# Optimization experiments

Measured on AMD Instinct MI355X. Metric: run time of the kernel, lower is better.

Reference implementation:

```python
import jax, jax.numpy as jnp
import numpy as np

D = 32        # number of TT cores (d)
R = 16        # tt_rank
B = 262144    # batch size


def setup_inputs() -> dict:
    key = jax.random.key(0)
    k1, k2, k3, k4 = jax.random.split(key, 4)
    return {
        "X": jax.random.randint(k1, (B, D), 0, 2, dtype=jnp.int32),
        "core_first": jax.random.normal(k2, (1, R, 2), dtype=jnp.float32),
        "cores_mid": jax.random.normal(k3, (D - 2, R, R, 2), dtype=jnp.float32),
        "core_last": jax.random.normal(k4, (R, 1, 2), dtype=jnp.float32),
    }


def reference(X, core_first, cores_mid, core_last):
    # First core: cores[0][:, :, X[:,0]] -> [1, R, B] -> permute -> [B, 1, R].
    # We carry the squeezed [B, R] row vector instead of [B, 1, R].
    carry0 = jnp.take(core_first[0], X[:, 0], axis=-1).T  # [B, R]

    def step(carry, inp):
        core, idx = inp                       # core: [R, R, 2], idx: [B]
        c = jnp.take(core, idx, axis=2)       # gathered core: [R, R, B]
        new = jnp.einsum('br,rsb->bs', carry, c)  # batched (1xR)@(RxR)
        return new, None

    # Middle cores i = 1 .. D-2 (sequential chain, data-dependent).
    carry, _ = jax.lax.scan(step, carry0, (cores_mid, X[:, 1:D - 1].T))

    # Last core: cores[-1][:, :, X[:,-1]] -> [R, 1, B]; contract to scalar per batch.
    c_last = jnp.take(core_last[:, 0, :], X[:, -1], axis=-1)  # [R, B]
    out = jnp.einsum('br,rb->b', carry, c_last)               # [B]  (squeeze of [B,1,1])
    return out
```

## Files before the change

kernel.cpp:

```cpp
#include <hip/hip_runtime.h>


#define R 16
#define TT_D 32
#define BATCH 262144

#define OFF_V16  0
#define OFF_W16  1048576
#define WS_FLOATS 2097152

#define MSTRIDE 268
#define VSTRIDE 17

__device__ __forceinline__ void rowvec_mat(const float* __restrict__ M,
                                           float* __restrict__ u) {
    float nv[R];
    #pragma unroll
    for (int s = 0; s < R; s++) nv[s] = 0.f;
    #pragma unroll
    for (int t2 = 0; t2 < R; t2++) {
        const float a = u[t2];
        #pragma unroll
        for (int s = 0; s < R; s++) nv[s] += a * M[t2 * 16 + s];
    }
    #pragma unroll
    for (int s = 0; s < R; s++) u[s] = nv[s];
}

__device__ __forceinline__ void mat_colvec(const float* __restrict__ M,
                                           float* __restrict__ w) {
    float nw[R];
    #pragma unroll
    for (int r2 = 0; r2 < R; r2++) {
        float a = 0.f;
        #pragma unroll
        for (int k = 0; k < R; k++) a += M[r2 * 16 + k] * w[k];
        nw[r2] = a;
    }
    #pragma unroll
    for (int r2 = 0; r2 < R; r2++) w[r2] = nw[r2];
}

__device__ __forceinline__ void chain4_row(const float* __restrict__ scm, int lbase,
                                           int e, int r, float* __restrict__ u) {
    const float* M0 = scm + lbase * 512 + ((e >> 3) & 1) * 256;
    #pragma unroll
    for (int s = 0; s < R; s++) u[s] = M0[r * 16 + s];
    for (int k = 1; k <= 3; k++) {
        const float* M = scm + (lbase + k) * 512 + ((e >> (3 - k)) & 1) * 256;
        rowvec_mat(M, u);
    }
}

__global__ __launch_bounds__(256) void tt_build(const float* __restrict__ cf,
                                                const float* __restrict__ cm,
                                                const float* __restrict__ cl,
                                                float* __restrict__ ws) {
    __shared__ float scm[15 * 512];
    __shared__ float T0[16 * MSTRIDE];
    __shared__ float T1[16 * MSTRIDE];
    __shared__ float SA[16 * VSTRIDE];
    __shared__ float SE[16 * VSTRIDE];
    __shared__ float SV[16];
    __shared__ float SG[256];

    const int t = threadIdx.x;
    const int e = t >> 4, r = t & 15;
    const bool isPrefix = (blockIdx.x < 256);
    const int h = isPrefix ? blockIdx.x : (blockIdx.x - 256);

    {
        const float2* cm2 = (const float2*)(cm + (isPrefix ? 0 : 15) * 512);
        for (int j = t; j < 15 * 256; j += 256) {
            const float2 vv = cm2[j];
            const int ci = j >> 8, idx = j & 255;
            scm[ci * 512 + idx] = vv.x;
            scm[ci * 512 + 256 + idx] = vv.y;
        }
    }
    __syncthreads();

    if (isPrefix) {
        if (t < 16) {
            SV[t] = cf[t * 2 + ((h >> 7) & 1)];
            for (int j = 0; j < 7; j++) {
                const float* M = scm + j * 512 + (((h >> (6 - j)) & 1) << 8);
                float a = 0.f;
                #pragma unroll
                for (int t2 = 0; t2 < R; t2++) a += SV[t2] * M[t2 * 16 + t];
                SV[t] = a;
            }
        }
        {
            float u[R];
            for (int tab = 0; tab < 2; tab++) {
                chain4_row(scm, 7 + 4 * tab, e, r, u);
                float* dst = (tab ? T1 : T0) + e * MSTRIDE + r * 16;
                #pragma unroll
                for (int s = 0; s < R; s++) dst[s] = u[s];
            }
        }
        __syncthreads();
        float v[R];
        #pragma unroll
        for (int k = 0; k < R; k++) v[k] = SV[k];
        const float* src = T0 + (t >> 4) * MSTRIDE;
        for (int q = 0; q < 2; q++) {
            rowvec_mat(src, v);
            src = T1 + (t & 15) * MSTRIDE;
        }
        float* o = ws + OFF_V16 + (size_t)(h * 256 + t) * 16;
        #pragma unroll
        for (int s = 0; s < R; s++) o[s] = v[s];
    } else {
        {
            float u[R];
            for (int job = 0; job < 2; job++) {
                int lb, ee, rr;
                float* dst;
                bool active = true;
                if (job == 0)      { lb = 8; ee = e;      rr = r;      dst = T0 + e * MSTRIDE + r * 16; }
                else if (t < 16)   { lb = 0; ee = h >> 4; rr = t;      dst = SA + t * VSTRIDE; }
                else if (t < 32)   { lb = 4; ee = h & 15; rr = t - 16; dst = SE + (t - 16) * VSTRIDE; }
                else               { active = false; lb = 0; ee = 0; rr = 0; dst = nullptr; }
                if (active) {
                    chain4_row(scm, lb, ee, rr, u);
                    #pragma unroll
                    for (int s = 0; s < R; s++) dst[s] = u[s];
                }
            }
        }
        if (t >= 48 && t < 64) {
            const int l = t - 48;
            float w[R];
            #pragma unroll
            for (int r2 = 0; r2 < R; r2++) w[r2] = cl[r2 * 2 + (l & 1)];
            for (int k = 0; k < 3; k++) {
                const float* M = scm + (14 - k) * 512 + (((l >> (k + 1)) & 1) << 8);
                mat_colvec(M, w);
            }
            float* dst = T1 + l * VSTRIDE;
            #pragma unroll
            for (int r2 = 0; r2 < R; r2++) dst[r2] = w[r2];
        }
        __syncthreads();
        {
            const int gr = t >> 4, gc = t & 15;
            float a = 0.f;
            #pragma unroll
            for (int k = 0; k < R; k++) a += SA[gr * VSTRIDE + k] * SE[k * VSTRIDE + gc];
            SG[gr * 16 + gc] = a;
        }
        __syncthreads();
        float w[R];
        #pragma unroll
        for (int k = 0; k < R; k++) w[k] = T1[(t & 15) * VSTRIDE + k];
        const float* src = T0 + (t >> 4) * MSTRIDE;
        for (int q = 0; q < 2; q++) {
            mat_colvec(src, w);
            src = SG;
        }
        float* o = ws + OFF_W16 + (size_t)(h * 256 + t) * 16;
        #pragma unroll
        for (int r2 = 0; r2 < R; r2++) o[r2] = w[r2];
    }
}

__global__ __launch_bounds__(256) void tt_main(const int* __restrict__ X,
                                               const float* __restrict__ ws,
                                               float* __restrict__ out) {
    const int b = blockIdx.x * 256 + threadIdx.x;
    const int4* Xr = (const int4*)(X + (size_t)b * TT_D);
    int xv[TT_D];
    #pragma unroll
    for (int q = 0; q < 8; q++) {
        int4 c = Xr[q];
        xv[q * 4 + 0] = c.x; xv[q * 4 + 1] = c.y; xv[q * 4 + 2] = c.z; xv[q * 4 + 3] = c.w;
    }
    unsigned p = 0, s = 0;
    #pragma unroll
    for (int i = 0; i < 16; i++) p = (p << 1) | (unsigned)(xv[i] & 1);
    #pragma unroll
    for (int i = 16; i < 32; i++) s = (s << 1) | (unsigned)(xv[i] & 1);

    const float4* v = (const float4*)(ws + OFF_V16 + (size_t)p * 16);
    const float4* w = (const float4*)(ws + OFF_W16 + (size_t)s * 16);
    float acc = 0.f;
    #pragma unroll
    for (int k = 0; k < 4; k++) {
        float4 a = v[k], c = w[k];
        acc += a.x * c.x + a.y * c.y + a.z * c.z + a.w * c.w;
    }
    out[b] = acc;
}

__global__ __launch_bounds__(256) void tt_direct(const int* __restrict__ X,
                                                 const float* __restrict__ cf,
                                                 const float* __restrict__ cm,
                                                 const float* __restrict__ cl,
                                                 float* __restrict__ out) {
    __shared__ float scm[30 * 16 * 16 * 2];
    for (int i = threadIdx.x; i < 30 * 16 * 16 * 2; i += blockDim.x) scm[i] = cm[i];
    __syncthreads();
    const int b = blockIdx.x * blockDim.x + threadIdx.x;
    if (b >= BATCH) return;
    const int* xr = X + (size_t)b * TT_D;
    float v[R], nv[R];
    const int x0 = xr[0] & 1;
    #pragma unroll
    for (int rr = 0; rr < R; rr++) v[rr] = cf[rr * 2 + x0];
    for (int i = 1; i <= 30; i++) {
        const int bit = xr[i] & 1;
        const float* M = scm + (i - 1) * 512;
        #pragma unroll
        for (int s2 = 0; s2 < R; s2++) {
            float acc = 0.f;
            #pragma unroll
            for (int rr = 0; rr < R; rr++) acc += v[rr] * M[(rr * 16 + s2) * 2 + bit];
            nv[s2] = acc;
        }
        #pragma unroll
        for (int s2 = 0; s2 < R; s2++) v[s2] = nv[s2];
    }
    const int xl = xr[31] & 1;
    float acc = 0.f;
    #pragma unroll
    for (int rr = 0; rr < R; rr++) acc += v[rr] * cl[rr * 2 + xl];
    out[b] = acc;
}

extern "C" void kernel_launch(void* const* d_in, const int* in_sizes, int n_in,
                              void* d_out, int out_size, void* d_ws, size_t ws_size,
                              hipStream_t stream) {
    const int* X = (const int*)d_in[0];
    const float* cf = (const float*)d_in[1];
    const float* cm = (const float*)d_in[2];
    const float* cl = (const float*)d_in[3];
    float* out = (float*)d_out;

    if (ws_size >= (size_t)WS_FLOATS * sizeof(float)) {
        float* ws = (float*)d_ws;
        tt_build<<<512, 256, 0, stream>>>(cf, cm, cl, ws);
        tt_main<<<BATCH / 256, 256, 0, stream>>>(X, ws, out);
    } else {
        tt_direct<<<(BATCH + 255) / 256, 256, 0, stream>>>(X, cf, cm, cl, out);
    }
}
```

Before: 112.1 us.

## Split table build into two stages and overlap X bit-packing with small-table build

The prefix/suffix table construction is split into two steps. A first kernel builds 8-core partial product tables (P8, Q8, V8, W8) in 34 blocks, while the remaining blocks pack each row of X into a 32-bit index. A second kernel combines these into the 16-bit prefix and suffix tables with a single matrix-vector product per entry, and a final gather kernel reads only the packed index. This removes the heavy per-block chain recomputation and hides the X read behind the table build. The cost is an extra kernel launch and extra workspace round-trips for the intermediate tables.

```diff
diff --git a/kernel.cpp b/kernel.cpp
--- a/kernel.cpp
+++ b/kernel.cpp
@@ -7,10 +7,15 @@
 
 #define OFF_V16  0
 #define OFF_W16  1048576
-#define WS_FLOATS 2097152
-
-#define MSTRIDE 268
-#define VSTRIDE 17
+#define OFF_P8   2097152
+#define OFF_Q8   (OFF_P8 + 65536)
+#define OFF_V8   (OFF_Q8 + 65536)
+#define OFF_W8   (OFF_V8 + 4096)
+#define OFF_PK   (OFF_W8 + 4096)
+#define WS_FLOATS (OFF_PK + BATCH)
+
+#define NBLK1 1024
+#define NTAB  34
 
 __device__ __forceinline__ void rowvec_mat(const float* __restrict__ M,
                                            float* __restrict__ u) {
@@ -41,154 +46,126 @@
     for (int r2 = 0; r2 < R; r2++) w[r2] = nw[r2];
 }
 
-__device__ __forceinline__ void chain4_row(const float* __restrict__ scm, int lbase,
-                                           int e, int r, float* __restrict__ u) {
-    const float* M0 = scm + lbase * 512 + ((e >> 3) & 1) * 256;
-    #pragma unroll
-    for (int s = 0; s < R; s++) u[s] = M0[r * 16 + s];
-    for (int k = 1; k <= 3; k++) {
-        const float* M = scm + (lbase + k) * 512 + ((e >> (3 - k)) & 1) * 256;
-        rowvec_mat(M, u);
-    }
-}
-
-__global__ __launch_bounds__(256) void tt_build(const float* __restrict__ cf,
-                                                const float* __restrict__ cm,
-                                                const float* __restrict__ cl,
-                                                float* __restrict__ ws) {
-    __shared__ float scm[15 * 512];
-    __shared__ float T0[16 * MSTRIDE];
-    __shared__ float T1[16 * MSTRIDE];
-    __shared__ float SA[16 * VSTRIDE];
-    __shared__ float SE[16 * VSTRIDE];
-    __shared__ float SV[16];
-    __shared__ float SG[256];
-
+__global__ __launch_bounds__(256) void tt_stage1(const int* __restrict__ X,
+                                                 const float* __restrict__ cf,
+                                                 const float* __restrict__ cm,
+                                                 const float* __restrict__ cl,
+                                                 float* __restrict__ ws) {
+    __shared__ float scm[8 * 512];
+    const int blk = blockIdx.x;
     const int t = threadIdx.x;
-    const int e = t >> 4, r = t & 15;
-    const bool isPrefix = (blockIdx.x < 256);
-    const int h = isPrefix ? blockIdx.x : (blockIdx.x - 256);
-
-    {
-        const float2* cm2 = (const float2*)(cm + (isPrefix ? 0 : 15) * 512);
-        for (int j = t; j < 15 * 256; j += 256) {
+
+    if (blk < NTAB) {
+        int cbase, ncore;
+        if (blk < 16)       { cbase = 7;  ncore = 8; }
+        else if (blk < 32)  { cbase = 15; ncore = 8; }
+        else if (blk == 32) { cbase = 0;  ncore = 7; }
+        else                { cbase = 23; ncore = 7; }
+        const float2* cm2 = (const float2*)(cm + cbase * 512);
+        for (int j = t; j < ncore * 256; j += 256) {
             const float2 vv = cm2[j];
             const int ci = j >> 8, idx = j & 255;
             scm[ci * 512 + idx] = vv.x;
             scm[ci * 512 + 256 + idx] = vv.y;
         }
-    }
-    __syncthreads();
-
-    if (isPrefix) {
-        if (t < 16) {
-            SV[t] = cf[t * 2 + ((h >> 7) & 1)];
-            for (int j = 0; j < 7; j++) {
-                const float* M = scm + j * 512 + (((h >> (6 - j)) & 1) << 8);
-                float a = 0.f;
-                #pragma unroll
-                for (int t2 = 0; t2 < R; t2++) a += SV[t2] * M[t2 * 16 + t];
-                SV[t] = a;
+        __syncthreads();
+
+        if (blk < 32) {
+            const bool isP = (blk < 16);
+            const int e = (isP ? blk : blk - 16) * 16 + (t >> 4), r = t & 15;
+            float u[R];
+            const float* M0 = scm + ((e >> 7) & 1) * 256;
+            #pragma unroll
+            for (int s = 0; s < R; s++) u[s] = M0[r * 16 + s];
+            for (int k = 1; k < 8; k++)
+                rowvec_mat(scm + k * 512 + ((e >> (7 - k)) & 1) * 256, u);
+            float* o = ws + (isP ? OFF_P8 : OFF_Q8) + e * 256 + r * 16;
+            #pragma unroll
+            for (int s = 0; s < R; s++) o[s] = u[s];
+        } else if (blk == 32) {
+            const int e = t;
+            float u[R];
+            #pragma unroll
+            for (int s = 0; s < R; s++) u[s] = cf[s * 2 + ((e >> 7) & 1)];
+            for (int k = 0; k < 7; k++)
+                rowvec_mat(scm + k * 512 + ((e >> (6 - k)) & 1) * 256, u);
+            float* o = ws + OFF_V8 + e * 16;
+            #pragma unroll
+            for (int s = 0; s < R; s++) o[s] = u[s];
+        } else {
+            const int e = t;
+            float w[R];
+            #pragma unroll
+            for (int r2 = 0; r2 < R; r2++) w[r2] = cl[r2 * 2 + (e & 1)];
+            for (int j = 6; j >= 0; j--)
+                mat_colvec(scm + j * 512 + ((e >> (7 - j)) & 1) * 256, w);
+            float* o = ws + OFF_W8 + e * 16;
+            #pragma unroll
+            for (int r2 = 0; r2 < R; r2++) o[r2] = w[r2];
+        }
+    } else {
+        unsigned* pk = (unsigned*)(ws + OFF_PK);
+        const int stride = (NBLK1 - NTAB) * 256;
+        for (int b = (blk - NTAB) * 256 + t; b < BATCH; b += stride) {
+            const int4* Xr = (const int4*)(X + (size_t)b * TT_D);
+            unsigned p = 0, s = 0;
+            #pragma unroll
+            for (int q = 0; q < 4; q++) {
+                const int4 c = Xr[q];
+                p = (p << 4) | ((unsigned)(c.x & 1) << 3) | ((unsigned)(c.y & 1) << 2)
+                             | ((unsigned)(c.z & 1) << 1) | (unsigned)(c.w & 1);
             }
-        }
-        {
-            float u[R];
-            for (int tab = 0; tab < 2; tab++) {
-                chain4_row(scm, 7 + 4 * tab, e, r, u);
-                float* dst = (tab ? T1 : T0) + e * MSTRIDE + r * 16;
-                #pragma unroll
-                for (int s = 0; s < R; s++) dst[s] = u[s];
+            #pragma unroll
+            for (int q = 4; q < 8; q++) {
+                const int4 c = Xr[q];
+                s = (s << 4) | ((unsigned)(c.x & 1) << 3) | ((unsigned)(c.y & 1) << 2)
+                             | ((unsigned)(c.z & 1) << 1) | (unsigned)(c.w & 1);
             }
-        }
-        __syncthreads();
-        float v[R];
-        #pragma unroll
-        for (int k = 0; k < R; k++) v[k] = SV[k];
-        const float* src = T0 + (t >> 4) * MSTRIDE;
-        for (int q = 0; q < 2; q++) {
-            rowvec_mat(src, v);
-            src = T1 + (t & 15) * MSTRIDE;
-        }
-        float* o = ws + OFF_V16 + (size_t)(h * 256 + t) * 16;
-        #pragma unroll
-        for (int s = 0; s < R; s++) o[s] = v[s];
+            pk[b] = (p << 16) | s;
+        }
+    }
+}
+
+__global__ __launch_bounds__(256) void tt_stage2(float* __restrict__ ws) {
+    __shared__ float sQ[256];
+    const int blk = blockIdx.x;
+    const int t = threadIdx.x;
+    if (blk < 256) {
+        const int hi = blk, lo = t;
+        float u[R];
+        const float* v8 = ws + OFF_V8 + hi * 16;
+        #pragma unroll
+        for (int k = 0; k < R; k++) u[k] = v8[k];
+        rowvec_mat(ws + OFF_P8 + lo * 256, u);
+        float* o = ws + OFF_V16 + (size_t)(hi * 256 + lo) * 16;
+        #pragma unroll
+        for (int s = 0; s < R; s++) o[s] = u[s];
     } else {
-        {
-            float u[R];
-            for (int job = 0; job < 2; job++) {
-                int lb, ee, rr;
-                float* dst;
-                bool active = true;
-                if (job == 0)      { lb = 8; ee = e;      rr = r;      dst = T0 + e * MSTRIDE + r * 16; }
-                else if (t < 16)   { lb = 0; ee = h >> 4; rr = t;      dst = SA + t * VSTRIDE; }
-                else if (t < 32)   { lb = 4; ee = h & 15; rr = t - 16; dst = SE + (t - 16) * VSTRIDE; }
-                else               { active = false; lb = 0; ee = 0; rr = 0; dst = nullptr; }
-                if (active) {
-                    chain4_row(scm, lb, ee, rr, u);
-                    #pragma unroll
-                    for (int s = 0; s < R; s++) dst[s] = u[s];
-                }
-            }
-        }
-        if (t >= 48 && t < 64) {
-            const int l = t - 48;
-            float w[R];
-            #pragma unroll
-            for (int r2 = 0; r2 < R; r2++) w[r2] = cl[r2 * 2 + (l & 1)];
-            for (int k = 0; k < 3; k++) {
-                const float* M = scm + (14 - k) * 512 + (((l >> (k + 1)) & 1) << 8);
-                mat_colvec(M, w);
-            }
-            float* dst = T1 + l * VSTRIDE;
-            #pragma unroll
-            for (int r2 = 0; r2 < R; r2++) dst[r2] = w[r2];
-        }
-        __syncthreads();
-        {
-            const int gr = t >> 4, gc = t & 15;
-            float a = 0.f;
-            #pragma unroll
-            for (int k = 0; k < R; k++) a += SA[gr * VSTRIDE + k] * SE[k * VSTRIDE + gc];
-            SG[gr * 16 + gc] = a;
-        }
+        const int hi = blk - 256, lo = t;
+        sQ[t] = ws[OFF_Q8 + hi * 256 + t];
         __syncthreads();
         float w[R];
-        #pragma unroll
-        for (int k = 0; k < R; k++) w[k] = T1[(t & 15) * VSTRIDE + k];
-        const float* src = T0 + (t >> 4) * MSTRIDE;
-        for (int q = 0; q < 2; q++) {
-            mat_colvec(src, w);
-            src = SG;
-        }
-        float* o = ws + OFF_W16 + (size_t)(h * 256 + t) * 16;
+        const float* w8 = ws + OFF_W8 + lo * 16;
+        #pragma unroll
+        for (int k = 0; k < R; k++) w[k] = w8[k];
+        mat_colvec(sQ, w);
+        float* o = ws + OFF_W16 + (size_t)(hi * 256 + lo) * 16;
         #pragma unroll
         for (int r2 = 0; r2 < R; r2++) o[r2] = w[r2];
     }
 }
 
-__global__ __launch_bounds__(256) void tt_main(const int* __restrict__ X,
-                                               const float* __restrict__ ws,
-                                               float* __restrict__ out) {
+__global__ __launch_bounds__(256) void tt_gather(const float* __restrict__ ws,
+                                                 float* __restrict__ out) {
     const int b = blockIdx.x * 256 + threadIdx.x;
-    const int4* Xr = (const int4*)(X + (size_t)b * TT_D);
-    int xv[TT_D];
-    #pragma unroll
-    for (int q = 0; q < 8; q++) {
-        int4 c = Xr[q];
-        xv[q * 4 + 0] = c.x; xv[q * 4 + 1] = c.y; xv[q * 4 + 2] = c.z; xv[q * 4 + 3] = c.w;
-    }
-    unsigned p = 0, s = 0;
-    #pragma unroll
-    for (int i = 0; i < 16; i++) p = (p << 1) | (unsigned)(xv[i] & 1);
-    #pragma unroll
-    for (int i = 16; i < 32; i++) s = (s << 1) | (unsigned)(xv[i] & 1);
-
+    const unsigned pk = ((const unsigned*)(ws + OFF_PK))[b];
+    const unsigned p = pk >> 16, s = pk & 0xffffu;
     const float4* v = (const float4*)(ws + OFF_V16 + (size_t)p * 16);
     const float4* w = (const float4*)(ws + OFF_W16 + (size_t)s * 16);
     float acc = 0.f;
     #pragma unroll
     for (int k = 0; k < 4; k++) {
-        float4 a = v[k], c = w[k];
+        const float4 a = v[k], c = w[k];
         acc += a.x * c.x + a.y * c.y + a.z * c.z + a.w * c.w;
     }
     out[b] = acc;
@@ -240,8 +217,9 @@
 
     if (ws_size >= (size_t)WS_FLOATS * sizeof(float)) {
         float* ws = (float*)d_ws;
-        tt_build<<<512, 256, 0, stream>>>(cf, cm, cl, ws);
-        tt_main<<<BATCH / 256, 256, 0, stream>>>(X, ws, out);
+        tt_stage1<<<NBLK1, 256, 0, stream>>>(X, cf, cm, cl, ws);
+        tt_stage2<<<512, 256, 0, stream>>>(ws);
+        tt_gather<<<BATCH / 256, 256, 0, stream>>>(ws, out);
     } else {
         tt_direct<<<(BATCH + 255) / 256, 256, 0, stream>>>(X, cf, cm, cl, out);
     }
```

Result: slower. 117.4 us (+4.8%).

## Pack X bit-indices inside the build kernel and gather from packed indices

Applied to the files above, without the earlier changes.

Moves the reading of X (32 ints per row, 32 MB) and its packing into a 32-bit index from the gather kernel into the table-build kernel. Each build block packs 512 rows before starting its table computation, and the packed indices go to an extra workspace region. The gather kernel then reads one uint per element instead of 128 bytes. The aim is to overlap the X streaming with the compute-bound table build, at the cost of a larger workspace requirement (which may push execution onto the fallback path if the workspace is too small) and a longer build kernel.

```diff
diff --git a/kernel.cpp b/kernel.cpp
--- a/kernel.cpp
+++ b/kernel.cpp
@@ -7,7 +7,8 @@
 
 #define OFF_V16  0
 #define OFF_W16  1048576
-#define WS_FLOATS 2097152
+#define OFF_PK   2097152
+#define WS_FLOATS (OFF_PK + BATCH)
 
 #define MSTRIDE 268
 #define VSTRIDE 17
@@ -52,10 +53,24 @@
     }
 }
 
-__global__ __launch_bounds__(256) void tt_build(const float* __restrict__ cf,
-                                                const float* __restrict__ cm,
-                                                const float* __restrict__ cl,
-                                                float* __restrict__ ws) {
+__device__ __forceinline__ unsigned pack_elem(const int* __restrict__ X, int b) {
+    const int4* Xr = (const int4*)(X + (size_t)b * TT_D);
+    unsigned v = 0;
+    #pragma unroll
+    for (int q = 0; q < 8; q++) {
+        const int4 c = Xr[q];
+        v = (v << 4) | ((unsigned)(c.x & 1) << 3) | ((unsigned)(c.y & 1) << 2)
+                     | ((unsigned)(c.z & 1) << 1) | (unsigned)(c.w & 1);
+    }
+    return v;
+}
+
+__global__ __launch_bounds__(256) void tt_build_pack(const int* __restrict__ X,
+                                                     const float* __restrict__ cf,
+                                                     const float* __restrict__ cm,
+                                                     const float* __restrict__ cl,
+                                                     float* __restrict__ ws,
+                                                     unsigned* __restrict__ pk) {
     __shared__ float scm[15 * 512];
     __shared__ float T0[16 * MSTRIDE];
     __shared__ float T1[16 * MSTRIDE];
@@ -68,6 +83,12 @@
     const int e = t >> 4, r = t & 15;
     const bool isPrefix = (blockIdx.x < 256);
     const int h = isPrefix ? blockIdx.x : (blockIdx.x - 256);
+
+    {
+        const int base = (int)blockIdx.x * 512;
+        pk[base + t]       = pack_elem(X, base + t);
+        pk[base + 256 + t] = pack_elem(X, base + 256 + t);
+    }
 
     {
         const float2* cm2 = (const float2*)(cm + (isPrefix ? 0 : 15) * 512);
@@ -166,29 +187,17 @@
     }
 }
 
-__global__ __launch_bounds__(256) void tt_main(const int* __restrict__ X,
-                                               const float* __restrict__ ws,
-                                               float* __restrict__ out) {
+__global__ __launch_bounds__(256) void tt_gather(const float* __restrict__ ws,
+                                                 const unsigned* __restrict__ pk,
+                                                 float* __restrict__ out) {
     const int b = blockIdx.x * 256 + threadIdx.x;
-    const int4* Xr = (const int4*)(X + (size_t)b * TT_D);
-    int xv[TT_D];
-    #pragma unroll
-    for (int q = 0; q < 8; q++) {
-        int4 c = Xr[q];
-        xv[q * 4 + 0] = c.x; xv[q * 4 + 1] = c.y; xv[q * 4 + 2] = c.z; xv[q * 4 + 3] = c.w;
-    }
-    unsigned p = 0, s = 0;
-    #pragma unroll
-    for (int i = 0; i < 16; i++) p = (p << 1) | (unsigned)(xv[i] & 1);
-    #pragma unroll
-    for (int i = 16; i < 32; i++) s = (s << 1) | (unsigned)(xv[i] & 1);
-
-    const float4* v = (const float4*)(ws + OFF_V16 + (size_t)p * 16);
-    const float4* w = (const float4*)(ws + OFF_W16 + (size_t)s * 16);
+    const unsigned v2 = pk[b];
+    const float4* v = (const float4*)(ws + OFF_V16 + (size_t)(v2 >> 16) * 16);
+    const float4* w = (const float4*)(ws + OFF_W16 + (size_t)(v2 & 0xffffu) * 16);
     float acc = 0.f;
     #pragma unroll
     for (int k = 0; k < 4; k++) {
-        float4 a = v[k], c = w[k];
+        const float4 a = v[k], c = w[k];
         acc += a.x * c.x + a.y * c.y + a.z * c.z + a.w * c.w;
     }
     out[b] = acc;
@@ -240,8 +249,9 @@
 
     if (ws_size >= (size_t)WS_FLOATS * sizeof(float)) {
         float* ws = (float*)d_ws;
-        tt_build<<<512, 256, 0, stream>>>(cf, cm, cl, ws);
-        tt_main<<<BATCH / 256, 256, 0, stream>>>(X, ws, out);
+        unsigned* pk = (unsigned*)(ws + OFF_PK);
+        tt_build_pack<<<512, 256, 0, stream>>>(X, cf, cm, cl, ws, pk);
+        tt_gather<<<BATCH / 256, 256, 0, stream>>>(ws, pk, out);
     } else {
         tt_direct<<<(BATCH + 255) / 256, 256, 0, stream>>>(X, cf, cm, cl, out);
     }
```

Result: no change. 111.8 us (-0.3%).
